# Kernel optimization log

Measured on AMD Instinct MI355X. Metric: run time of the kernel, lower is better.

## Reference

```python
import jax, jax.numpy as jnp
import numpy as np

# --- batched state-vector quantum circuit sim: AngleEmbedding(RY) + BasicEntanglerLayers(RX + ring CNOT) ---

def _ry(state, theta, wire, n):
    # per-sample RY(theta) on `wire`; state: (B,) + (2,)*n complex
    ax = wire + 1
    c = jnp.cos(0.5 * theta).reshape((-1,) + (1,) * (n - 1)).astype(state.dtype)
    s = jnp.sin(0.5 * theta).reshape((-1,) + (1,) * (n - 1)).astype(state.dtype)
    s0 = jnp.take(state, 0, axis=ax)
    s1 = jnp.take(state, 1, axis=ax)
    return jnp.stack([c * s0 - s * s1, s * s0 + c * s1], axis=ax)

def _rx(state, theta, wire, n):
    # scalar RX(theta) on `wire` (shared weight across batch)
    ax = wire + 1
    c = jnp.cos(0.5 * theta).astype(state.dtype)
    s = (-1j * jnp.sin(0.5 * theta)).astype(state.dtype)
    s0 = jnp.take(state, 0, axis=ax)
    s1 = jnp.take(state, 1, axis=ax)
    return jnp.stack([c * s0 + s * s1, s * s0 + c * s1], axis=ax)

def _cnot(state, ctrl, tgt):
    ax_c = ctrl + 1
    s0 = jnp.take(state, 0, axis=ax_c)
    s1 = jnp.take(state, 1, axis=ax_c)
    ax_t = tgt + 1 if tgt < ctrl else tgt  # target axis index after removing ctrl axis
    s1 = jnp.flip(s1, axis=ax_t)
    return jnp.stack([s0, s1], axis=ax_c)

def _circuit(x_qin, qweights):
    # x_qin: (Bn, n) angles; qweights: (L, n)
    Bn, n = x_qin.shape
    state = jnp.zeros((Bn,) + (2,) * n, jnp.complex64)
    state = state.at[(slice(None),) + (0,) * n].set(1.0)
    for w in range(n):  # AngleEmbedding, rotation='Y'
        state = _ry(state, x_qin[:, w], w, n)
    for l in range(qweights.shape[0]):  # BasicEntanglerLayers
        for w in range(n):
            state = _rx(state, qweights[l, w], w, n)
        for w in range(n):
            state = _cnot(state, w, (w + 1) % n)
    probs = jnp.real(state * jnp.conj(state))
    outs = []
    for w in range(n):  # <Z_w> = P(bit_w=0) - P(bit_w=1)
        axes = tuple(a for a in range(1, n + 1) if a != w + 1)
        p = probs.sum(axis=axes)  # (Bn, 2)
        outs.append(p[:, 0] - p[:, 1])
    return jnp.stack(outs, axis=-1).astype(jnp.float32)


def setup_inputs() -> dict:
    key = jax.random.key(0)
    ks = jax.random.split(key, 9)
    B, N, H, NQ, L = 16, 1024, 256, 8, 2
    x = jax.random.normal(ks[0], (B, N, H), jnp.float32)
    norm_adj = jax.random.uniform(ks[1], (N, N), jnp.float32) / N
    Wg = jax.random.normal(ks[2], (H, H), jnp.float32) * 0.02
    bg = jax.random.normal(ks[3], (H,), jnp.float32) * 0.02
    Wpre = jax.random.normal(ks[4], (NQ, H), jnp.float32) * 0.05
    bpre = jax.random.normal(ks[5], (NQ,), jnp.float32) * 0.02
    qweights = jax.random.uniform(ks[6], (L, NQ), jnp.float32) * (2.0 * np.pi)
    Wpost = jax.random.normal(ks[7], (H, NQ), jnp.float32) * 0.1
    bpost = jax.random.normal(ks[8], (H,), jnp.float32) * 0.02
    return {"x": x, "norm_adj": norm_adj, "Wg": Wg, "bg": bg, "Wpre": Wpre,
            "bpre": bpre, "qweights": qweights, "Wpost": Wpost, "bpost": bpost}


def reference(x, norm_adj, Wg, bg, Wpre, bpre, qweights, Wpost, bpost):
    # GCN aggregation + GELU(Linear)  (dropout is identity in eval mode)
    x_agg = jnp.einsum('ij,bjh->bih', norm_adj, x)
    x_agg = jax.nn.gelu(x_agg @ Wg.T + bg, approximate=False)
    B, N, H = x_agg.shape
    x_flat = x_agg.reshape(B * N, H).astype(jnp.float32)
    x_qin = jnp.tanh(x_flat @ Wpre.T + bpre) * np.pi
    q_out = _circuit(x_qin, qweights)          # (B*N, n_qubits)
    out = (q_out @ Wpost.T + bpost).reshape(B, N, H)
    return out
```

## Files before the change

### kernel.cpp

```cpp
#include <hip/hip_runtime.h>
#include <math.h>

typedef __attribute__((ext_vector_type(8))) short bf16x8;
typedef _Float16 f16x8 __attribute__((ext_vector_type(8)));
typedef __attribute__((ext_vector_type(4))) float f32x4;

#define PI_F 3.14159265358979323846f

__device__ __forceinline__ unsigned short f2bf(float f) {
  unsigned int u = __float_as_uint(f);
  u += 0x7FFFu + ((u >> 16) & 1u);
  return (unsigned short)(u >> 16);
}

__device__ __forceinline__ float bf2f(unsigned short u) {
  return __uint_as_float(((unsigned int)u) << 16);
}

__device__ __forceinline__ void async_ld16(const unsigned short* g, unsigned short* l) {
  __builtin_amdgcn_global_load_lds(
      (const __attribute__((address_space(1))) void*)g,
      (__attribute__((address_space(3))) void*)l,
      16, 0, 0);
}

__device__ __forceinline__ float fast_erf(float x) {
  float a = fabsf(x);
  float t = 1.0f / fmaf(0.3275911f, a, 1.0f);
  float p = t * fmaf(t, fmaf(t, fmaf(t, fmaf(t, 1.061405429f, -1.453152027f),
                                     1.421413741f), -0.284496736f), 0.254829592f);
  float e = __expf(-a * a);
  float r = 1.0f - p * e;
  return copysignf(r, x);
}

__device__ __forceinline__ float fast_tanh(float a) {
  float e = __expf(2.0f * a);
  return 1.0f - 2.0f / (e + 1.0f);
}

template<int ML, int MR>
__device__ __forceinline__ void apply_rx(float re[4], float im[4], float c, float s) {
  float pr[4], pi[4];
  #pragma unroll
  for (int r = 0; r < 4; r++) {
    float vr = re[r ^ MR], vi = im[r ^ MR];
    if (ML) { vr = __shfl_xor(vr, ML, 64); vi = __shfl_xor(vi, ML, 64); }
    pr[r] = vr; pi[r] = vi;
  }
  #pragma unroll
  for (int r = 0; r < 4; r++) {
    re[r] = fmaf(c, re[r],  s * pi[r]);
    im[r] = fmaf(c, im[r], -s * pr[r]);
  }
}

__global__ __launch_bounds__(256)
void prep_kernel(const float* __restrict__ adj, unsigned short* __restrict__ adj_bf,
                 const float* __restrict__ Wg, unsigned short* __restrict__ Wg_bf,
                 const float* __restrict__ qw, unsigned short* __restrict__ Uri,
                 const float* __restrict__ Wpost, _Float16* __restrict__ Gt,
                 const float* __restrict__ x, unsigned short* __restrict__ xT) {
  __shared__ float smem[1056];
  int bid = blockIdx.x, t = threadIdx.x;
  if (bid < 1024) {
    int i = bid * 256 + t;
    float4 v = ((const float4*)adj)[i];
    ushort4 o; o.x = f2bf(v.x); o.y = f2bf(v.y); o.z = f2bf(v.z); o.w = f2bf(v.w);
    ((ushort4*)adj_bf)[i] = o;
  } else if (bid < 1088) {
    int i = (bid - 1024) * 256 + t;
    float4 v = ((const float4*)Wg)[i];
    ushort4 o; o.x = f2bf(v.x); o.y = f2bf(v.y); o.z = f2bf(v.z); o.w = f2bf(v.w);
    ((ushort4*)Wg_bf)[i] = o;
  } else if (bid < 1152) {
    if (t < 16) { smem[t] = cosf(0.5f * qw[t]); smem[16 + t] = sinf(0.5f * qw[t]); }
    __syncthreads();
    int wv = t >> 6, L = t & 63;
    int k = (bid - 1088) * 4 + wv;
    float re[4], im[4];
    #pragma unroll
    for (int r = 0; r < 4; r++) { re[r] = (r * 64 + L == k) ? 1.f : 0.f; im[r] = 0.f; }
    apply_rx<1, 0>(re, im, smem[0], smem[16]);
    apply_rx<2, 0>(re, im, smem[1], smem[17]);
    apply_rx<4, 0>(re, im, smem[2], smem[18]);
    apply_rx<8, 0>(re, im, smem[3], smem[19]);
    apply_rx<16, 0>(re, im, smem[4], smem[20]);
    apply_rx<32, 0>(re, im, smem[5], smem[21]);
    apply_rx<0, 1>(re, im, smem[6], smem[22]);
    apply_rx<0, 2>(re, im, smem[7], smem[23]);
    apply_rx<3, 0>(re, im, smem[8], smem[24]);
    apply_rx<6, 0>(re, im, smem[9], smem[25]);
    apply_rx<12, 0>(re, im, smem[10], smem[26]);
    apply_rx<24, 0>(re, im, smem[11], smem[27]);
    apply_rx<48, 0>(re, im, smem[12], smem[28]);
    apply_rx<32, 1>(re, im, smem[13], smem[29]);
    apply_rx<0, 3>(re, im, smem[14], smem[30]);
    apply_rx<3, 2>(re, im, smem[15], smem[31]);
    const int M[8] = {0xAB, 0xFD, 0xFA, 0xF5, 0xEA, 0xD5, 0xAA, 0x55};
    #pragma unroll
    for (int r = 0; r < 4; r++) {
      int n = 0;
      #pragma unroll
      for (int w = 0; w < 8; w++) {
        int bit = (__popc(L & (M[w] & 63)) ^ __popc((r << 6) & M[w])) & 1;
        n |= bit << w;
      }
      int row_re = ((n >> 4) << 5) + (n & 15);
      Uri[(size_t)row_re * 256 + k] = f2bf(re[r]);
      Uri[(size_t)(row_re + 16) * 256 + k] = f2bf(im[r]);
    }
  } else if (bid < 1168) {
    int tid = (bid - 1152) * 256 + t;
    int h = tid >> 4;
    int n0 = (tid & 15) << 4;
    float wv8[8];
    #pragma unroll
    for (int w = 0; w < 8; w++) wv8[w] = Wpost[h * 8 + w];
    #pragma unroll
    for (int j = 0; j < 16; j++) {
      int n = n0 + j;
      float sum = 0.f;
      #pragma unroll
      for (int w = 0; w < 8; w++) sum += ((n >> w) & 1) ? -wv8[w] : wv8[w];
      Gt[h * 256 + n] = (_Float16)sum;
    }
  } else {
    int tb = bid - 1168;
    int jt = tb & 31, ht = (tb >> 5) & 7, bb = tb >> 8;
    const float* xb = x + (size_t)bb * 1024 * 256;
    int row = t >> 3, cg = t & 7;
    {
      float4 v = *(const float4*)&xb[(size_t)(jt * 32 + row) * 256 + ht * 32 + cg * 4];
      smem[row * 33 + cg * 4 + 0] = v.x;
      smem[row * 33 + cg * 4 + 1] = v.y;
      smem[row * 33 + cg * 4 + 2] = v.z;
      smem[row * 33 + cg * 4 + 3] = v.w;
    }
    __syncthreads();
    unsigned short* xTb = xT + (size_t)bb * 256 * 1024;
    int h = ht * 32 + row;
    ushort4 o;
    o.x = f2bf(smem[(cg * 4 + 0) * 33 + row]);
    o.y = f2bf(smem[(cg * 4 + 1) * 33 + row]);
    o.z = f2bf(smem[(cg * 4 + 2) * 33 + row]);
    o.w = f2bf(smem[(cg * 4 + 3) * 33 + row]);
    *(ushort4*)&xTb[(size_t)h * 1024 + jt * 32 + cg * 4] = o;
  }
}

__global__ __launch_bounds__(256)
void gemm1_kernel(const unsigned short* __restrict__ A,
                  const unsigned short* __restrict__ Bt,
                  unsigned short* __restrict__ C,
                  int K, int tilesN, int ldC) {
  __shared__ unsigned short As[2 * 2 * 128 * 32];
  __shared__ unsigned short Bs[2 * 2 * 128 * 32];
  int bid = blockIdx.x;
  int swz = (bid & 7) * 32 + (bid >> 3);
  int in_ = swz >> 3;
  int im  = swz & 7;
  const unsigned short* Ab  = A  + (long long)im * 128 * K;
  const unsigned short* Btb = Bt + (long long)in_ * 128 * K;

  int t = threadIdx.x;
  int wv = t >> 6, lane = t & 63;
  int wm = wv >> 1, wn = wv & 1;
  int l15 = lane & 15, quad = lane >> 4;

  int r0 = t >> 2,         c0 = (t & 3) ^ ((r0 >> 1) & 3);
  int r1 = (256 + t) >> 2, c1 = (t & 3) ^ ((r1 >> 1) & 3);
  long long go0 = (long long)r0 * K + c0 * 8;
  long long go1 = (long long)r1 * K + c1 * 8;

  f32x4 acc[4][4] = {};

  #pragma unroll
  for (int kb = 0; kb < 2; kb++) {
    async_ld16(Ab + go0 + kb * 32, &As[kb * 4096 + t * 8]);
    async_ld16(Ab + go1 + kb * 32, &As[kb * 4096 + (256 + t) * 8]);
    async_ld16(Btb + go0 + kb * 32, &Bs[kb * 4096 + t * 8]);
    async_ld16(Btb + go1 + kb * 32, &Bs[kb * 4096 + (256 + t) * 8]);
  }
  __syncthreads();

  int nk = K >> 6;
  for (int ki = 0; ki < nk; ki++) {
    int buf = ki & 1;
    if (ki + 1 < nk) {
      int nb = buf ^ 1;
      long long kk = (long long)(ki + 1) << 6;
      #pragma unroll
      for (int kb = 0; kb < 2; kb++) {
        async_ld16(Ab + go0 + kk + kb * 32, &As[nb * 8192 + kb * 4096 + t * 8]);
        async_ld16(Ab + go1 + kk + kb * 32, &As[nb * 8192 + kb * 4096 + (256 + t) * 8]);
        async_ld16(Btb + go0 + kk + kb * 32, &Bs[nb * 8192 + kb * 4096 + t * 8]);
        async_ld16(Btb + go1 + kk + kb * 32, &Bs[nb * 8192 + kb * 4096 + (256 + t) * 8]);
      }
    }
    #pragma unroll
    for (int kb = 0; kb < 2; kb++) {
      bf16x8 af[4], bfr[4];
      #pragma unroll
      for (int mt = 0; mt < 4; mt++) {
        int row = wm * 64 + mt * 16 + l15;
        af[mt] = *(const bf16x8*)&As[buf * 8192 + kb * 4096 + row * 32 +
                                     ((quad ^ ((row >> 1) & 3)) * 8)];
      }
      #pragma unroll
      for (int nt = 0; nt < 4; nt++) {
        int row = wn * 64 + nt * 16 + l15;
        bfr[nt] = *(const bf16x8*)&Bs[buf * 8192 + kb * 4096 + row * 32 +
                                      ((quad ^ ((row >> 1) & 3)) * 8)];
      }
      #pragma unroll
      for (int mt = 0; mt < 4; mt++)
        #pragma unroll
        for (int nt = 0; nt < 4; nt++)
          acc[mt][nt] = __builtin_amdgcn_mfma_f32_16x16x32_bf16(af[mt], bfr[nt], acc[mt][nt], 0, 0, 0);
    }
    __syncthreads();
  }

  int n0 = in_ * 128;
  #pragma unroll
  for (int mt = 0; mt < 4; mt++) {
    #pragma unroll
    for (int nt = 0; nt < 4; nt++) {
      int colg = n0 + wn * 64 + nt * 16 + l15;
      #pragma unroll
      for (int r = 0; r < 4; r++) {
        int rowg = im * 128 + wm * 64 + mt * 16 + quad * 4 + r;
        C[(size_t)rowg * ldC + colg] = f2bf(acc[mt][nt][r]);
      }
    }
  }
}

__global__ __launch_bounds__(1024, 4)
void qfused_kernel(const unsigned short* __restrict__ xagg,
                   const unsigned short* __restrict__ Wg,
                   const float* __restrict__ bg,
                   const float* __restrict__ Wpre, const float* __restrict__ bpre,
                   const unsigned short* __restrict__ Uri,
                   const _Float16* __restrict__ Gt,
                   const float* __restrict__ bpost,
                   float* __restrict__ out) {
  __shared__ __align__(16) char smemraw[102400];
  unsigned short* As  = (unsigned short*)smemraw;
  unsigned short* gs  = (unsigned short*)(smemraw + 32768);
  _Float16*       Ts  = (_Float16*)(smemraw + 32768);
  unsigned short* P0s = (unsigned short*)(smemraw + 65536);
  float*          prt = (float*)(smemraw + 65536);
  float*          csw = (float*)(smemraw + 98304);

  int t = threadIdx.x;
  int wv = t >> 6, lane = t & 63;
  int l15 = lane & 15, quad = lane >> 4;

  const unsigned short* Ab = xagg + (size_t)blockIdx.x * 64 * 256;

  #pragma unroll
  for (int q = 0; q < 2; q++) {
    int sidx = q * 1024 + t;
    int kb = sidx >> 8;
    int r  = (sidx >> 2) & 63;
    int c  = (sidx & 3) ^ ((r >> 1) & 3);
    async_ld16(Ab + (size_t)r * 256 + kb * 32 + c * 8, &As[sidx * 8]);
  }
  const unsigned short* Wp = Wg + (size_t)(wv * 16 + l15) * 256 + quad * 8;
  bf16x8 wf[8];
  #pragma unroll
  for (int k8 = 0; k8 < 8; k8++) wf[k8] = *(const bf16x8*)(Wp + k8 * 32);
  __syncthreads();

  f32x4 acc[4] = {};
  #pragma unroll
  for (int k8 = 0; k8 < 8; k8++) {
    #pragma unroll
    for (int mt = 0; mt < 4; mt++) {
      int row = mt * 16 + l15;
      bf16x8 af = *(const bf16x8*)&As[k8 * 2048 + row * 32 + ((quad ^ ((row >> 1) & 3)) * 8)];
      acc[mt] = __builtin_amdgcn_mfma_f32_16x16x32_bf16(af, wf[k8], acc[mt], 0, 0, 0);
    }
  }
  {
    int col = wv * 16 + l15;
    float bgl = bg[col];
    int kbc = col >> 5, chunk = (col >> 3) & 3, e = col & 7;
    #pragma unroll
    for (int mt = 0; mt < 4; mt++) {
      #pragma unroll
      for (int r = 0; r < 4; r++) {
        int row = mt * 16 + quad * 4 + r;
        float v = acc[mt][r] + bgl;
        v = 0.5f * v * (1.0f + fast_erf(v * 0.7071067811865475f));
        *(unsigned short*)((char*)gs + kbc * 4096 + row * 64 +
                           ((chunk ^ ((row >> 1) & 3)) << 4) + e * 2) = f2bf(v);
      }
    }
  }
  __syncthreads();

  {
    int k8 = wv >> 1, mh = wv & 1;
    const float* wrow = Wpre + (size_t)(l15 & 7) * 256 + k8 * 32 + quad * 8;
    float4 wa = *(const float4*)wrow;
    float4 wb = *(const float4*)(wrow + 4);
    float v8[8] = {wa.x, wa.y, wa.z, wa.w, wb.x, wb.y, wb.z, wb.w};
    bf16x8 whi, wlo;
    #pragma unroll
    for (int j = 0; j < 8; j++) {
      unsigned short h = f2bf(v8[j]);
      whi[j] = (short)h;
      wlo[j] = (short)f2bf(v8[j] - bf2f(h));
    }
    f32x4 aacc[2] = {};
    #pragma unroll
    for (int mt = 0; mt < 2; mt++) {
      int row = mh * 32 + mt * 16 + l15;
      bf16x8 ga = *(const bf16x8*)((char*)gs + k8 * 4096 + row * 64 +
                                   ((quad ^ ((row >> 1) & 3)) << 4));
      aacc[mt] = __builtin_amdgcn_mfma_f32_16x16x32_bf16(ga, whi, aacc[mt], 0, 0, 0);
      aacc[mt] = __builtin_amdgcn_mfma_f32_16x16x32_bf16(ga, wlo, aacc[mt], 0, 0, 0);
    }
    if (l15 < 8) {
      #pragma unroll
      for (int mt = 0; mt < 2; mt++)
        #pragma unroll
        for (int r = 0; r < 4; r++)
          prt[k8 * 512 + (mh * 32 + mt * 16 + quad * 4 + r) * 8 + l15] = aacc[mt][r];
    }
  }
  __syncthreads();

  if (t < 512) {
    float s = 0.f;
    #pragma unroll
    for (int k = 0; k < 8; k++) s += prt[k * 512 + t];
    float th = (0.5f * PI_F) * fast_tanh(s + bpre[t & 7]);
    int row = t >> 3, w = t & 7;
    csw[row * 16 + w] = __cosf(th);
    csw[row * 16 + 8 + w] = __sinf(th);
  }
  __syncthreads();

  #pragma unroll
  for (int rr = 0; rr < 4; rr++) {
    int row = wv * 4 + rr;
    float4 c0 = *(const float4*)&csw[row * 16];
    float4 c1 = *(const float4*)&csw[row * 16 + 4];
    float4 s0 = *(const float4*)&csw[row * 16 + 8];
    float4 s1 = *(const float4*)&csw[row * 16 + 12];
    float cw[8] = {c0.x, c0.y, c0.z, c0.w, c1.x, c1.y, c1.z, c1.w};
    float sw[8] = {s0.x, s0.y, s0.z, s0.w, s1.x, s1.y, s1.z, s1.w};
    float pl = 1.f;
    #pragma unroll
    for (int b = 0; b < 6; b++) pl *= ((lane >> b) & 1) ? sw[b + 2] : cw[b + 2];
    ushort4 o;
    o.x = f2bf(pl * cw[0] * cw[1]);
    o.y = f2bf(pl * sw[0] * cw[1]);
    o.z = f2bf(pl * cw[0] * sw[1]);
    o.w = f2bf(pl * sw[0] * sw[1]);
    int jj = lane & 7;
    int cswz = (jj >> 1) ^ ((row >> 1) & 3);
    *(ushort4*)((char*)P0s + (lane >> 3) * 4096 + row * 64 + cswz * 16 + (jj & 1) * 8) = o;
  }
  const unsigned short* Up = Uri + (size_t)(wv * 32 + l15) * 256 + quad * 8;
  bf16x8 ua[2][2];
  #pragma unroll
  for (int sl = 0; sl < 2; sl++)
    #pragma unroll
    for (int nt = 0; nt < 2; nt++)
      ua[sl][nt] = *(const bf16x8*)(Up + sl * 32 + nt * 4096);
  __syncthreads();

  f32x4 acc1[4][2] = {};
  {
    #pragma unroll
    for (int k8 = 0; k8 < 8; k8++) {
      int cur = k8 & 1;
      #pragma unroll
      for (int mt = 0; mt < 4; mt++) {
        int row = mt * 16 + l15;
        bf16x8 pa = *(const bf16x8*)((char*)P0s + k8 * 4096 + row * 64 +
                                     ((quad ^ ((row >> 1) & 3)) << 4));
        acc1[mt][0] = __builtin_amdgcn_mfma_f32_16x16x32_bf16(pa, ua[cur][0], acc1[mt][0], 0, 0, 0);
        acc1[mt][1] = __builtin_amdgcn_mfma_f32_16x16x32_bf16(pa, ua[cur][1], acc1[mt][1], 0, 0, 0);
      }
      if (k8 < 6) {
        #pragma unroll
        for (int nt = 0; nt < 2; nt++)
          ua[cur][nt] = *(const bf16x8*)(Up + (k8 + 2) * 32 + nt * 4096);
      }
    }
  }

  {
    int colT = wv * 16 + l15;
    int kbc = colT >> 5, chunk = (colT >> 3) & 3, e = colT & 7;
    #pragma unroll
    for (int mt = 0; mt < 4; mt++) {
      #pragma unroll
      for (int r = 0; r < 4; r++) {
        int row = mt * 16 + quad * 4 + r;
        float tre = acc1[mt][0][r], tim = acc1[mt][1][r];
        *(_Float16*)((char*)Ts + kbc * 4096 + row * 64 +
                     ((chunk ^ ((row >> 1) & 3)) << 4) + e * 2)
            = (_Float16)(tre * tre + tim * tim);
      }
    }
  }
  const _Float16* Gp = Gt + (size_t)(wv * 16 + l15) * 256 + quad * 8;
  f16x8 gf[2];
  gf[0] = *(const f16x8*)(Gp);
  gf[1] = *(const f16x8*)(Gp + 32);
  __syncthreads();

  f32x4 acc2[4] = {};
  {
    #pragma unroll
    for (int k8 = 0; k8 < 8; k8++) {
      int cur = k8 & 1;
      #pragma unroll
      for (int mt = 0; mt < 4; mt++) {
        int row = mt * 16 + l15;
        f16x8 tf = *(const f16x8*)((char*)Ts + k8 * 4096 + row * 64 +
                                   ((quad ^ ((row >> 1) & 3)) << 4));
        acc2[mt] = __builtin_amdgcn_mfma_f32_16x16x32_f16(tf, gf[cur], acc2[mt], 0, 0, 0);
      }
      if (k8 < 6) gf[cur] = *(const f16x8*)(Gp + (k8 + 2) * 32);
    }
  }

  {
    int col = wv * 16 + l15;
    float bp = bpost[col];
    #pragma unroll
    for (int mt = 0; mt < 4; mt++) {
      #pragma unroll
      for (int r = 0; r < 4; r++) {
        int row = mt * 16 + quad * 4 + r;
        int s = blockIdx.x * 64 + row;
        int orow = (s & 15) * 1024 + (s >> 4);
        out[(size_t)orow * 256 + col] = acc2[mt][r] + bp;
      }
    }
  }
}

extern "C" void kernel_launch(void* const* d_in, const int* in_sizes, int n_in,
                              void* d_out, int out_size, void* d_ws, size_t ws_size,
                              hipStream_t stream) {
  const float* x     = (const float*)d_in[0];
  const float* adj   = (const float*)d_in[1];
  const float* Wg    = (const float*)d_in[2];
  const float* bg    = (const float*)d_in[3];
  const float* Wpre  = (const float*)d_in[4];
  const float* bpre  = (const float*)d_in[5];
  const float* qw    = (const float*)d_in[6];
  const float* Wpost = (const float*)d_in[7];
  const float* bpost = (const float*)d_in[8];
  float* out = (float*)d_out;

  char* ws = (char*)d_ws;
  unsigned short* adj_bf  = (unsigned short*)(ws + 0);
  unsigned short* Wg_bf   = (unsigned short*)(ws + 2097152);
  unsigned short* xT_bf   = (unsigned short*)(ws + 2228224);
  unsigned short* xagg_bf = (unsigned short*)(ws + 10616832);
  unsigned short* Uri     = (unsigned short*)(ws + 19005440);
  _Float16*       Gt      = (_Float16*)(ws + 19267584);

  prep_kernel<<<5264, 256, 0, stream>>>(adj, adj_bf, Wg, Wg_bf, qw, Uri,
                                        Wpost, Gt, x, xT_bf);

  gemm1_kernel<<<256, 256, 0, stream>>>(adj_bf, xT_bf, xagg_bf, 1024, 32, 4096);

  qfused_kernel<<<256, 1024, 0, stream>>>(xagg_bf, Wg_bf, bg, Wpre, bpre, Uri, Gt, bpost, out);
}
```

Measured before the change: 133.4 us.

## Spread gemm1 128x128 tile over 16 waves instead of 4

```diff
diff --git a/kernel.cpp b/kernel.cpp
--- a/kernel.cpp
+++ b/kernel.cpp
@@ -149,13 +149,12 @@
   }
 }
 
-__global__ __launch_bounds__(256)
+__global__ __launch_bounds__(1024)
 void gemm1_kernel(const unsigned short* __restrict__ A,
                   const unsigned short* __restrict__ Bt,
                   unsigned short* __restrict__ C,
                   int K, int tilesN, int ldC) {
-  __shared__ unsigned short As[2 * 2 * 128 * 32];
-  __shared__ unsigned short Bs[2 * 2 * 128 * 32];
+  __shared__ unsigned short Ss[2 * 2 * 2 * 128 * 32];
   int bid = blockIdx.x;
   int swz = (bid & 7) * 32 + (bid >> 3);
   int in_ = swz >> 3;
@@ -165,23 +164,20 @@
 
   int t = threadIdx.x;
   int wv = t >> 6, lane = t & 63;
-  int wm = wv >> 1, wn = wv & 1;
+  int wm = wv >> 2, wn = wv & 3;
   int l15 = lane & 15, quad = lane >> 4;
 
-  int r0 = t >> 2,         c0 = (t & 3) ^ ((r0 >> 1) & 3);
-  int r1 = (256 + t) >> 2, c1 = (t & 3) ^ ((r1 >> 1) & 3);
-  long long go0 = (long long)r0 * K + c0 * 8;
-  long long go1 = (long long)r1 * K + c1 * 8;
-
-  f32x4 acc[4][4] = {};
-
-  #pragma unroll
-  for (int kb = 0; kb < 2; kb++) {
-    async_ld16(Ab + go0 + kb * 32, &As[kb * 4096 + t * 8]);
-    async_ld16(Ab + go1 + kb * 32, &As[kb * 4096 + (256 + t) * 8]);
-    async_ld16(Btb + go0 + kb * 32, &Bs[kb * 4096 + t * 8]);
-    async_ld16(Btb + go1 + kb * 32, &Bs[kb * 4096 + (256 + t) * 8]);
-  }
+  int isB = t >> 9;
+  int s0  = t & 511;
+  int r0  = s0 >> 2, c0 = (s0 & 3) ^ ((r0 >> 1) & 3);
+  const unsigned short* Gb = isB ? Btb : Ab;
+  long long go = (long long)r0 * K + c0 * 8;
+
+  f32x4 acc[2][2] = {};
+
+  #pragma unroll
+  for (int kb = 0; kb < 2; kb++)
+    async_ld16(Gb + go + kb * 32, &Ss[(isB * 2 + kb) * 4096 + s0 * 8]);
   __syncthreads();
 
   int nk = K >> 6;
@@ -191,32 +187,29 @@
       int nb = buf ^ 1;
       long long kk = (long long)(ki + 1) << 6;
       #pragma unroll
-      for (int kb = 0; kb < 2; kb++) {
-        async_ld16(Ab + go0 + kk + kb * 32, &As[nb * 8192 + kb * 4096 + t * 8]);
-        async_ld16(Ab + go1 + kk + kb * 32, &As[nb * 8192 + kb * 4096 + (256 + t) * 8]);
-        async_ld16(Btb + go0 + kk + kb * 32, &Bs[nb * 8192 + kb * 4096 + t * 8]);
-        async_ld16(Btb + go1 + kk + kb * 32, &Bs[nb * 8192 + kb * 4096 + (256 + t) * 8]);
-      }
+      for (int kb = 0; kb < 2; kb++)
+        async_ld16(Gb + go + kk + kb * 32,
+                   &Ss[((nb * 2 + isB) * 2 + kb) * 4096 + s0 * 8]);
     }
     #pragma unroll
     for (int kb = 0; kb < 2; kb++) {
-      bf16x8 af[4], bfr[4];
-      #pragma unroll
-      for (int mt = 0; mt < 4; mt++) {
-        int row = wm * 64 + mt * 16 + l15;
-        af[mt] = *(const bf16x8*)&As[buf * 8192 + kb * 4096 + row * 32 +
-                                     ((quad ^ ((row >> 1) & 3)) * 8)];
-      }
-      #pragma unroll
-      for (int nt = 0; nt < 4; nt++) {
-        int row = wn * 64 + nt * 16 + l15;
-        bfr[nt] = *(const bf16x8*)&Bs[buf * 8192 + kb * 4096 + row * 32 +
-                                      ((quad ^ ((row >> 1) & 3)) * 8)];
-      }
-      #pragma unroll
-      for (int mt = 0; mt < 4; mt++)
+      const unsigned short* Sa = &Ss[((buf * 2 + 0) * 2 + kb) * 4096];
+      const unsigned short* Sb = &Ss[((buf * 2 + 1) * 2 + kb) * 4096];
+      bf16x8 af[2], bfr[2];
+      #pragma unroll
+      for (int mt = 0; mt < 2; mt++) {
+        int row = wm * 32 + mt * 16 + l15;
+        af[mt] = *(const bf16x8*)&Sa[row * 32 + ((quad ^ ((row >> 1) & 3)) * 8)];
+      }
+      #pragma unroll
+      for (int nt = 0; nt < 2; nt++) {
+        int row = wn * 32 + nt * 16 + l15;
+        bfr[nt] = *(const bf16x8*)&Sb[row * 32 + ((quad ^ ((row >> 1) & 3)) * 8)];
+      }
+      #pragma unroll
+      for (int mt = 0; mt < 2; mt++)
         #pragma unroll
-        for (int nt = 0; nt < 4; nt++)
+        for (int nt = 0; nt < 2; nt++)
           acc[mt][nt] = __builtin_amdgcn_mfma_f32_16x16x32_bf16(af[mt], bfr[nt], acc[mt][nt], 0, 0, 0);
     }
     __syncthreads();
@@ -224,13 +217,13 @@
 
   int n0 = in_ * 128;
   #pragma unroll
-  for (int mt = 0; mt < 4; mt++) {
-    #pragma unroll
-    for (int nt = 0; nt < 4; nt++) {
-      int colg = n0 + wn * 64 + nt * 16 + l15;
+  for (int mt = 0; mt < 2; mt++) {
+    #pragma unroll
+    for (int nt = 0; nt < 2; nt++) {
+      int colg = n0 + wn * 32 + nt * 16 + l15;
       #pragma unroll
       for (int r = 0; r < 4; r++) {
-        int rowg = im * 128 + wm * 64 + mt * 16 + quad * 4 + r;
+        int rowg = im * 128 + wm * 32 + mt * 16 + quad * 4 + r;
         C[(size_t)rowg * ldC + colg] = f2bf(acc[mt][nt][r]);
       }
     }
@@ -474,7 +467,7 @@
   prep_kernel<<<5264, 256, 0, stream>>>(adj, adj_bf, Wg, Wg_bf, qw, Uri,
                                         Wpost, Gt, x, xT_bf);
 
-  gemm1_kernel<<<256, 256, 0, stream>>>(adj_bf, xT_bf, xagg_bf, 1024, 32, 4096);
+  gemm1_kernel<<<256, 1024, 0, stream>>>(adj_bf, xT_bf, xagg_bf, 1024, 32, 4096);
 
   qfused_kernel<<<256, 1024, 0, stream>>>(xagg_bf, Wg_bf, bg, Wpre, bpre, Uri, Gt, bpost, out);
 }
```

Result: faster. 128.4 us (-3.7%).
